# Kernel optimization log

Measured on AMD Instinct MI355X. Metric: run time of the kernel, lower is better.

The kernel has to match this reference:

```python
import jax, jax.numpy as jnp
import numpy as np

BN_EPS = 1e-5


def setup_inputs() -> dict:
    key = jax.random.key(0)
    ks = jax.random.split(key, 8)
    N, C, H, W = 16, 64, 56, 56
    Ch = C // 2
    x = jax.random.normal(ks[0], (N, C, H, W), dtype=jnp.float32)
    # 1x1 convs represented as [out, in] matrices
    w1 = jax.random.normal(ks[1], (Ch, C), dtype=jnp.float32) / np.sqrt(C)
    b1 = jnp.zeros((Ch,), dtype=jnp.float32)
    w2 = jax.random.normal(ks[2], (Ch, C), dtype=jnp.float32) / np.sqrt(C)
    b2 = jnp.zeros((Ch,), dtype=jnp.float32)
    w3 = jax.random.normal(ks[3], (C, C), dtype=jnp.float32) / np.sqrt(C)
    b3 = jnp.zeros((C,), dtype=jnp.float32)
    gamma = jnp.ones((C,), dtype=jnp.float32)
    beta = jnp.zeros((C,), dtype=jnp.float32)
    return {"x": x, "w1": w1, "b1": b1, "w2": w2, "b2": b2,
            "w3": w3, "b3": b3, "gamma": gamma, "beta": beta}


def _conv1x1(x, w, b):
    # x: [N,C,H,W], w: [O,C] -> [N,O,H,W]
    return jnp.einsum('nchw,oc->nohw', x, w) + b[None, :, None, None]


def reference(x, w1, b1, w2, b2, w3, b3, gamma, beta):
    N, C, H, W = x.shape
    S = H * W
    theta = _conv1x1(x, w1, b1)            # [N, C/2, H, W]
    phi = _conv1x1(x, w2, b2)              # [N, C/2, H, W]
    g = x                                  # [N, C, H, W]
    th = theta.reshape(N, -1, S)           # [N, C/2, S]
    ph = phi.reshape(N, -1, S)             # [N, C/2, S]
    gf = g.reshape(N, C, S)                # [N, C, S]
    scale = 1.0 / jnp.sqrt(jnp.float32(th.shape[1]))
    attn = jnp.einsum('nis,nit->nst', th, ph) * scale   # [N, S, S]
    attn = jax.nn.softmax(attn, axis=-1)
    f = jnp.einsum('nst,nit->nis', attn, gf).reshape(N, C, H, W)
    f = _conv1x1(f, w3, b3)
    # BatchNorm2d, training mode (batch statistics, biased variance)
    mean = jnp.mean(f, axis=(0, 2, 3), keepdims=True)
    var = jnp.mean((f - mean) ** 2, axis=(0, 2, 3), keepdims=True)
    f = (f - mean) / jnp.sqrt(var + BN_EPS)
    f = f * gamma[None, :, None, None] + beta[None, :, None, None]
    return x + f
```

## Files before the change

kernel.cpp:

```cpp
#include <hip/hip_runtime.h>
#include <hip/hip_bf16.h>

constexpr int N_ = 16, C_ = 64, CH_ = 32;
constexpr int S_ = 3136;
constexpr int SB = 64;
constexpr int NB = S_ / SB;
constexpr float SCALE = 0.17677669529663687f;
constexpr float LOG2E = 1.4426950408889634f;
constexpr float SCALE2 = SCALE * LOG2E;
constexpr float FIXM2 = 16.0f * LOG2E;

using f32x4 = __attribute__((ext_vector_type(4))) float;
using f32x16 = __attribute__((ext_vector_type(16))) float;
using bf16x8 = __attribute__((ext_vector_type(8))) short;
using u32x2 = __attribute__((ext_vector_type(2))) unsigned;
using u32x4 = __attribute__((ext_vector_type(4))) unsigned;

__device__ __forceinline__ unsigned cvtpk(float lo, float hi) {
  unsigned r;
  asm("v_cvt_pk_bf16_f32 %0, %1, %2" : "=v"(r) : "v"(lo), "v"(hi));
  return r;
}
__device__ __forceinline__ float exp2a(float x) {
  float r;
  asm("v_exp_f32 %0, %1" : "=v"(r) : "v"(x));
  return r;
}
__device__ __forceinline__ unsigned short f2bf(float f) {
  unsigned int u = __builtin_bit_cast(unsigned int, f);
  u += 0x7fffu + ((u >> 16) & 1u);
  return (unsigned short)(u >> 16);
}

__global__ __launch_bounds__(256)
void prep_kernel(const float* __restrict__ x,
                 const float* __restrict__ w1, const float* __restrict__ b1,
                 const float* __restrict__ w2, const float* __restrict__ b2,
                 unsigned short* __restrict__ thetaT,
                 unsigned short* __restrict__ phiT,
                 unsigned short* __restrict__ xbf) {
  __shared__ float xl[64][68];
  __shared__ __align__(16) unsigned short thL[64][40];
  __shared__ __align__(16) unsigned short phL[64][40];
  const int b = blockIdx.x;
  const int n = b / NB;
  const int s0 = (b % NB) * SB;
  const int tid = threadIdx.x;
  const int sl = tid & 63;
  const int grp = tid >> 6;

#pragma unroll
  for (int cc = 0; cc < 4; ++cc) {
    int c = cc * 16 + grp * 4 + (sl >> 4);
    int s4 = (sl & 15) * 4;
    size_t gidx = (size_t)(n * C_ + c) * S_ + s0 + s4;
    f32x4 v = *(const f32x4*)(x + gidx);
    *(f32x4*)&xl[c][s4] = v;
    u32x2 pb;
    pb.x = cvtpk(v[0], v[1]);
    pb.y = cvtpk(v[2], v[3]);
    *(u32x2*)(xbf + gidx) = pb;
  }
  __syncthreads();

  float acc1[8], acc2[8];
  const int i0u = __builtin_amdgcn_readfirstlane(grp * 8);
  const float* w1b = w1 + i0u * C_;
  const float* w2b = w2 + i0u * C_;
#pragma unroll
  for (int ii = 0; ii < 8; ++ii) {
    acc1[ii] = b1[i0u + ii];
    acc2[ii] = b2[i0u + ii];
  }
#pragma unroll 1
  for (int cc = 0; cc < 4; ++cc) {
    float xv[16];
#pragma unroll
    for (int k = 0; k < 16; ++k) xv[k] = xl[cc * 16 + k][sl];
#pragma unroll
    for (int ii = 0; ii < 8; ++ii) {
#pragma unroll
      for (int k = 0; k < 16; ++k) {
        acc1[ii] = fmaf(w1b[ii * C_ + cc * 16 + k], xv[k], acc1[ii]);
        acc2[ii] = fmaf(w2b[ii * C_ + cc * 16 + k], xv[k], acc2[ii]);
      }
    }
  }
  {
    u32x4 t4, p4;
    t4.x = cvtpk(acc1[0] * SCALE2, acc1[1] * SCALE2);
    t4.y = cvtpk(acc1[2] * SCALE2, acc1[3] * SCALE2);
    t4.z = cvtpk(acc1[4] * SCALE2, acc1[5] * SCALE2);
    t4.w = cvtpk(acc1[6] * SCALE2, acc1[7] * SCALE2);
    p4.x = cvtpk(acc2[0], acc2[1]);
    p4.y = cvtpk(acc2[2], acc2[3]);
    p4.z = cvtpk(acc2[4], acc2[5]);
    p4.w = cvtpk(acc2[6], acc2[7]);
    *(u32x4*)&thL[sl][grp * 8] = t4;
    *(u32x4*)&phL[sl][grp * 8] = p4;
  }
  __syncthreads();
  {
    int row = tid >> 2, ch = (tid & 3) * 8;
    size_t o = ((size_t)(n * S_) + s0 + row) * CH_ + ch;
    *(bf16x8*)(thetaT + o) = *(const bf16x8*)&thL[row][ch];
    *(bf16x8*)(phiT + o)   = *(const bf16x8*)&phL[row][ch];
  }
}

__global__ __launch_bounds__(256)
void attn_kernel(const unsigned short* __restrict__ thetaT,
                 const unsigned short* __restrict__ phiT,
                 const unsigned short* __restrict__ xbf,
                 const float* __restrict__ w3, const float* __restrict__ b3,
                 unsigned short* __restrict__ yb, float* __restrict__ partials) {
  __shared__ __align__(16) unsigned short ldsK[2][64 * 40];
  __shared__ __align__(16) unsigned short ldsV[2][64 * 72];
  __shared__ float redS[2][128];
  const int b = (blockIdx.x & 7) * 98 + (blockIdx.x >> 3);
  const int n = b / NB;
  const int q0 = (b % NB) * SB;
  const int tid = threadIdx.x;
  const int lane = tid & 63;
  const int w = tid >> 6;
  const int qw = w & 1;
  const int th = w >> 1;
  const int cl = lane & 31;
  const int h = lane >> 5;

  const unsigned short* thQ =
      thetaT + ((size_t)(n * S_) + q0 + qw * 32 + cl) * CH_;
  const bf16x8 qfA = *(const bf16x8*)(thQ + h * 8);
  const bf16x8 qfB = *(const bf16x8*)(thQ + 16 + h * 8);

  f32x16 oacc[2];
#pragma unroll
  for (int cb = 0; cb < 2; ++cb)
#pragma unroll
    for (int r = 0; r < 16; ++r) oacc[cb][r] = 0.f;
  float lsum = 0.f;
  f32x16 cinit;
#pragma unroll
  for (int r = 0; r < 16; ++r) cinit[r] = -FIXM2;

  const unsigned short* phiB = phiT + (size_t)n * S_ * CH_;
  const unsigned short* vB = xbf + (size_t)n * C_ * S_;

  const int krow = tid >> 2, kch = (tid & 3) * 8;
  const int vc = tid >> 3, vch = (tid & 7) * 8;

  bf16x8 kst, vst0, vst1;
  kst = *(const bf16x8*)(phiB + (size_t)krow * CH_ + kch);
  vst0 = *(const bf16x8*)(vB + (size_t)vc * S_ + vch);
  vst1 = *(const bf16x8*)(vB + (size_t)(vc + 32) * S_ + vch);
  *(bf16x8*)(ldsK[0] + krow * 40 + kch) = kst;
  *(bf16x8*)(ldsV[0] + vc * 72 + vch) = vst0;
  *(bf16x8*)(ldsV[0] + (vc + 32) * 72 + vch) = vst1;
  __syncthreads();

  int cur = 0;
#pragma unroll 1
  for (int t0 = 0; t0 < S_; t0 += 64) {
    const bool pre = (t0 + 64 < S_);
    if (pre) {
      kst = *(const bf16x8*)(phiB + (size_t)(t0 + 64 + krow) * CH_ + kch);
      vst0 = *(const bf16x8*)(vB + (size_t)vc * S_ + t0 + 64 + vch);
      vst1 = *(const bf16x8*)(vB + (size_t)(vc + 32) * S_ + t0 + 64 + vch);
    }

    const unsigned short* Kc = ldsK[cur];
    const unsigned short* Vc = ldsV[cur];

    const unsigned short* kr = Kc + (th * 32 + cl) * 40 + h * 8;
    bf16x8 kfA = *(const bf16x8*)(kr);
    bf16x8 kfB = *(const bf16x8*)(kr + 16);
    __builtin_amdgcn_s_setprio(1);
    f32x16 st = __builtin_amdgcn_mfma_f32_32x32x16_bf16(kfA, qfA, cinit, 0, 0, 0);
    st = __builtin_amdgcn_mfma_f32_32x32x16_bf16(kfB, qfB, st, 0, 0, 0);
    __builtin_amdgcn_s_setprio(0);

    float p[16];
#pragma unroll
    for (int r = 0; r < 16; ++r) {
      p[r] = exp2a(st[r]);
      lsum += p[r];
    }
    unsigned pkw[8];
#pragma unroll
    for (int i = 0; i < 8; ++i) pkw[i] = cvtpk(p[2 * i], p[2 * i + 1]);

    __builtin_amdgcn_s_setprio(1);
#pragma unroll
    for (int tb = 0; tb < 2; ++tb) {
      bf16x8 pf = __builtin_bit_cast(bf16x8,
          (u32x4){pkw[tb * 4 + 0], pkw[tb * 4 + 1], pkw[tb * 4 + 2], pkw[tb * 4 + 3]});
#pragma unroll
      for (int cb = 0; cb < 2; ++cb) {
        const unsigned short* vr =
            Vc + (cb * 32 + cl) * 72 + th * 32 + tb * 16 + 4 * h;
        u32x2 v0 = *(const u32x2*)(vr);
        u32x2 v1 = *(const u32x2*)(vr + 8);
        bf16x8 vf = __builtin_bit_cast(bf16x8, (u32x4){v0.x, v0.y, v1.x, v1.y});
        oacc[cb] = __builtin_amdgcn_mfma_f32_32x32x16_bf16(vf, pf, oacc[cb], 0, 0, 0);
      }
    }
    __builtin_amdgcn_s_setprio(0);

    if (pre) {
      *(bf16x8*)(ldsK[cur ^ 1] + krow * 40 + kch) = kst;
      *(bf16x8*)(ldsV[cur ^ 1] + vc * 72 + vch) = vst0;
      *(bf16x8*)(ldsV[cur ^ 1] + (vc + 32) * 72 + vch) = vst1;
    }
    __syncthreads();
    cur ^= 1;
  }

  float* mrg = (float*)&ldsV[0][0];
  if (th == 1) {
    float* pm = mrg + ((size_t)(qw * 64 + lane)) * 36;
#pragma unroll
    for (int cb = 0; cb < 2; ++cb)
#pragma unroll
      for (int i = 0; i < 4; ++i) {
        f32x4 v = {oacc[cb][4 * i], oacc[cb][4 * i + 1],
                   oacc[cb][4 * i + 2], oacc[cb][4 * i + 3]};
        *(f32x4*)(pm + cb * 16 + 4 * i) = v;
      }
    pm[32] = lsum;
  }
  __syncthreads();
  if (th == 0) {
    float* pm = mrg + ((size_t)(qw * 64 + lane)) * 36;
#pragma unroll
    for (int cb = 0; cb < 2; ++cb)
#pragma unroll
      for (int i = 0; i < 4; ++i) {
        f32x4 v = *(const f32x4*)(pm + cb * 16 + 4 * i);
        oacc[cb][4 * i] += v[0];
        oacc[cb][4 * i + 1] += v[1];
        oacc[cb][4 * i + 2] += v[2];
        oacc[cb][4 * i + 3] += v[3];
      }
    lsum += pm[32];

    float lt = lsum;
    lt += __shfl_xor(lt, 32);
    const float inv = 1.0f / lt;

    unsigned ff[4][4];
#pragma unroll
    for (int kb = 0; kb < 4; ++kb) {
      const int blk = kb >> 1, rb = (kb & 1) * 8;
#pragma unroll
      for (int i = 0; i < 4; ++i)
        ff[kb][i] = cvtpk(oacc[blk][rb + 2 * i] * inv,
                          oacc[blk][rb + 2 * i + 1] * inv);
    }

    const int q = q0 + qw * 32 + cl;
#pragma unroll
    for (int ch32 = 0; ch32 < 2; ++ch32) {
      const float* wr = w3 + (ch32 * 32 + cl) * C_;
      f32x16 acc;
      {
        f32x4 b0 = *(const f32x4*)(b3 + ch32 * 32 + 4 * h);
        f32x4 b1v = *(const f32x4*)(b3 + ch32 * 32 + 8 + 4 * h);
        f32x4 b2v = *(const f32x4*)(b3 + ch32 * 32 + 16 + 4 * h);
        f32x4 b3v = *(const f32x4*)(b3 + ch32 * 32 + 24 + 4 * h);
#pragma unroll
        for (int i = 0; i < 4; ++i) {
          acc[i] = b0[i];
          acc[4 + i] = b1v[i];
          acc[8 + i] = b2v[i];
          acc[12 + i] = b3v[i];
        }
      }
#pragma unroll
      for (int kb = 0; kb < 4; ++kb) {
        f32x4 a0 = *(const f32x4*)(wr + kb * 16 + 4 * h);
        f32x4 a1 = *(const f32x4*)(wr + kb * 16 + 8 + 4 * h);
        u32x4 wf;
        wf.x = cvtpk(a0[0], a0[1]);
        wf.y = cvtpk(a0[2], a0[3]);
        wf.z = cvtpk(a1[0], a1[1]);
        wf.w = cvtpk(a1[2], a1[3]);
        bf16x8 fb = __builtin_bit_cast(bf16x8,
            (u32x4){ff[kb][0], ff[kb][1], ff[kb][2], ff[kb][3]});
        acc = __builtin_amdgcn_mfma_f32_32x32x16_bf16(
            __builtin_bit_cast(bf16x8, wf), fb, acc, 0, 0, 0);
      }
#pragma unroll
      for (int r = 0; r < 16; ++r) {
        const int co = ch32 * 32 + (r & 3) + 8 * (r >> 2) + 4 * h;
        float yv = acc[r];
        yb[(size_t)(n * C_ + co) * S_ + q] = f2bf(yv);
        float s1 = yv, s2 = yv * yv;
#pragma unroll
        for (int off = 1; off < 32; off <<= 1) {
          s1 += __shfl_xor(s1, off);
          s2 += __shfl_xor(s2, off);
        }
        if (cl == 0) {
          redS[qw][co] = s1;
          redS[qw][64 + co] = s2;
        }
      }
    }
  }
  __syncthreads();
  if (tid < 128)
    partials[(size_t)b * 128 + tid] = redS[0][tid] + redS[1][tid];
}

__global__ __launch_bounds__(256)
void stats_kernel(const float* __restrict__ partials, float* __restrict__ stats) {
  __shared__ float red[4];
  const int c = blockIdx.x;
  const int tid = threadIdx.x;
  float s = 0.f;
  for (int r = tid; r < N_ * NB; r += 256) s += partials[(size_t)r * 128 + c];
#pragma unroll
  for (int off = 1; off < 64; off <<= 1) s += __shfl_xor(s, off);
  if ((tid & 63) == 0) red[tid >> 6] = s;
  __syncthreads();
  if (tid == 0) stats[c] = red[0] + red[1] + red[2] + red[3];
}

__global__ __launch_bounds__(256)
void bn_kernel(const unsigned short* __restrict__ xbf,
               const unsigned short* __restrict__ yb,
               const float* __restrict__ stats,
               const float* __restrict__ gamma, const float* __restrict__ beta,
               float* __restrict__ out) {
  const int idx = blockIdx.x * 256 + threadIdx.x;
  const size_t base = (size_t)idx * 8;
  const int c = (int)((base / S_) & 63);
  constexpr float invcnt = 1.0f / (N_ * S_);
  float mean = stats[c] * invcnt;
  float var = stats[64 + c] * invcnt - mean * mean;
  float a = gamma[c] * rsqrtf(var + 1e-5f);
  float bb = beta[c] - mean * a;
  u32x4 yv = *(const u32x4*)(yb + base);
  u32x4 xv = *(const u32x4*)(xbf + base);
#pragma unroll
  for (int hh = 0; hh < 2; ++hh) {
    f32x4 o;
#pragma unroll
    for (int r = 0; r < 2; ++r) {
      const int wsel = hh * 2 + r;
      unsigned py = (wsel == 0) ? yv.x : (wsel == 1) ? yv.y : (wsel == 2) ? yv.z : yv.w;
      unsigned px = (wsel == 0) ? xv.x : (wsel == 1) ? xv.y : (wsel == 2) ? xv.z : xv.w;
      float ylo = __builtin_bit_cast(float, py << 16);
      float yhi = __builtin_bit_cast(float, py & 0xffff0000u);
      float xlo = __builtin_bit_cast(float, px << 16);
      float xhi = __builtin_bit_cast(float, px & 0xffff0000u);
      o[r * 2 + 0] = fmaf(ylo, a, xlo + bb);
      o[r * 2 + 1] = fmaf(yhi, a, xhi + bb);
    }
    *(f32x4*)(out + base + hh * 4) = o;
  }
}

extern "C" void kernel_launch(void* const* d_in, const int* in_sizes, int n_in,
                              void* d_out, int out_size, void* d_ws, size_t ws_size,
                              hipStream_t stream) {
  const float* x = (const float*)d_in[0];
  const float* w1 = (const float*)d_in[1];
  const float* b1 = (const float*)d_in[2];
  const float* w2 = (const float*)d_in[3];
  const float* b2 = (const float*)d_in[4];
  const float* w3 = (const float*)d_in[5];
  const float* b3 = (const float*)d_in[6];
  const float* gamma = (const float*)d_in[7];
  const float* beta = (const float*)d_in[8];

  char* ws = (char*)d_ws;
  unsigned short* thetaT = (unsigned short*)(ws + 0);
  unsigned short* phiT   = (unsigned short*)(ws + 3211264);
  unsigned short* xbf    = (unsigned short*)(ws + 6422528);
  unsigned short* yb     = (unsigned short*)(ws + 12845056);
  float* stats           = (float*)(ws + 19267584);
  float* partials        = (float*)(ws + 19268096);
  if (ws_size < 19669504) return;

  prep_kernel<<<N_ * NB, 256, 0, stream>>>(x, w1, b1, w2, b2, thetaT, phiT, xbf);
  attn_kernel<<<N_ * NB, 256, 0, stream>>>(thetaT, phiT, xbf, w3, b3, yb, partials);
  stats_kernel<<<128, 256, 0, stream>>>(partials, stats);
  bn_kernel<<<(out_size / 8) / 256, 256, 0, stream>>>(xbf, yb, stats, gamma, beta, (float*)d_out);
}
```

Measured before the change: 105.0 us.

## Load K and V fragments straight from global into registers, dropping LDS staging

The attention loop no longer stages phi (K) and x (V) tiles through double-buffered shared memory. Each lane now loads its MFMA fragments directly from global memory into registers, with a two-stage register ping-pong prefetch, which removes the per-iteration __syncthreads and the LDS traffic. The cost is more global load instructions with narrower 8-byte V accesses and redundant loads across waves, which now depend on L1/L2 hits. Register pressure also rises, which may lower occupancy.

```diff
diff --git a/kernel.cpp b/kernel.cpp
--- a/kernel.cpp
+++ b/kernel.cpp
@@ -114,8 +114,7 @@
                  const unsigned short* __restrict__ xbf,
                  const float* __restrict__ w3, const float* __restrict__ b3,
                  unsigned short* __restrict__ yb, float* __restrict__ partials) {
-  __shared__ __align__(16) unsigned short ldsK[2][64 * 40];
-  __shared__ __align__(16) unsigned short ldsV[2][64 * 72];
+  __shared__ float mrg[2][64][36];
   __shared__ float redS[2][128];
   const int b = (blockIdx.x & 7) * 98 + (blockIdx.x >> 3);
   const int n = b / NB;
@@ -143,42 +142,32 @@
 #pragma unroll
   for (int r = 0; r < 16; ++r) cinit[r] = -FIXM2;
 
-  const unsigned short* phiB = phiT + (size_t)n * S_ * CH_;
-  const unsigned short* vB = xbf + (size_t)n * C_ * S_;
-
-  const int krow = tid >> 2, kch = (tid & 3) * 8;
-  const int vc = tid >> 3, vch = (tid & 7) * 8;
-
-  bf16x8 kst, vst0, vst1;
-  kst = *(const bf16x8*)(phiB + (size_t)krow * CH_ + kch);
-  vst0 = *(const bf16x8*)(vB + (size_t)vc * S_ + vch);
-  vst1 = *(const bf16x8*)(vB + (size_t)(vc + 32) * S_ + vch);
-  *(bf16x8*)(ldsK[0] + krow * 40 + kch) = kst;
-  *(bf16x8*)(ldsV[0] + vc * 72 + vch) = vst0;
-  *(bf16x8*)(ldsV[0] + (vc + 32) * 72 + vch) = vst1;
-  __syncthreads();
-
-  int cur = 0;
-#pragma unroll 1
-  for (int t0 = 0; t0 < S_; t0 += 64) {
-    const bool pre = (t0 + 64 < S_);
-    if (pre) {
-      kst = *(const bf16x8*)(phiB + (size_t)(t0 + 64 + krow) * CH_ + kch);
-      vst0 = *(const bf16x8*)(vB + (size_t)vc * S_ + t0 + 64 + vch);
-      vst1 = *(const bf16x8*)(vB + (size_t)(vc + 32) * S_ + t0 + 64 + vch);
-    }
-
-    const unsigned short* Kc = ldsK[cur];
-    const unsigned short* Vc = ldsV[cur];
-
-    const unsigned short* kr = Kc + (th * 32 + cl) * 40 + h * 8;
-    bf16x8 kfA = *(const bf16x8*)(kr);
-    bf16x8 kfB = *(const bf16x8*)(kr + 16);
+  const unsigned short* kBase =
+      phiT + (size_t)n * S_ * CH_ + (size_t)(th * 32 + cl) * CH_ + h * 8;
+  const unsigned short* vBase =
+      xbf + (size_t)n * C_ * S_ + (size_t)cl * S_ + th * 32 + 4 * h;
+  const size_t vRow32 = (size_t)32 * S_;
+
+  bf16x8 kA0, kB0, kA1, kB1;
+  u32x2 VA[8], VB[8];
+
+  auto prefetch = [&](bf16x8& KA, bf16x8& KB, u32x2* VV, int t) {
+    const unsigned short* kp = kBase + (size_t)t * CH_;
+    KA = *(const bf16x8*)kp;
+    KB = *(const bf16x8*)(kp + 16);
+    const unsigned short* vp = vBase + t;
+#pragma unroll
+    for (int j = 0; j < 4; ++j) VV[j] = *(const u32x2*)(vp + j * 8);
+    const unsigned short* vp2 = vp + vRow32;
+#pragma unroll
+    for (int j = 0; j < 4; ++j) VV[4 + j] = *(const u32x2*)(vp2 + j * 8);
+  };
+
+  auto compute = [&](bf16x8 KA, bf16x8 KB, const u32x2* VV) {
     __builtin_amdgcn_s_setprio(1);
-    f32x16 st = __builtin_amdgcn_mfma_f32_32x32x16_bf16(kfA, qfA, cinit, 0, 0, 0);
-    st = __builtin_amdgcn_mfma_f32_32x32x16_bf16(kfB, qfB, st, 0, 0, 0);
+    f32x16 st = __builtin_amdgcn_mfma_f32_32x32x16_bf16(KA, qfA, cinit, 0, 0, 0);
+    st = __builtin_amdgcn_mfma_f32_32x32x16_bf16(KB, qfB, st, 0, 0, 0);
     __builtin_amdgcn_s_setprio(0);
-
     float p[16];
 #pragma unroll
     for (int r = 0; r < 16; ++r) {
@@ -188,7 +177,6 @@
     unsigned pkw[8];
 #pragma unroll
     for (int i = 0; i < 8; ++i) pkw[i] = cvtpk(p[2 * i], p[2 * i + 1]);
-
     __builtin_amdgcn_s_setprio(1);
 #pragma unroll
     for (int tb = 0; tb < 2; ++tb) {
@@ -196,28 +184,28 @@
           (u32x4){pkw[tb * 4 + 0], pkw[tb * 4 + 1], pkw[tb * 4 + 2], pkw[tb * 4 + 3]});
 #pragma unroll
       for (int cb = 0; cb < 2; ++cb) {
-        const unsigned short* vr =
-            Vc + (cb * 32 + cl) * 72 + th * 32 + tb * 16 + 4 * h;
-        u32x2 v0 = *(const u32x2*)(vr);
-        u32x2 v1 = *(const u32x2*)(vr + 8);
+        u32x2 v0 = VV[cb * 4 + tb * 2];
+        u32x2 v1 = VV[cb * 4 + tb * 2 + 1];
         bf16x8 vf = __builtin_bit_cast(bf16x8, (u32x4){v0.x, v0.y, v1.x, v1.y});
         oacc[cb] = __builtin_amdgcn_mfma_f32_32x32x16_bf16(vf, pf, oacc[cb], 0, 0, 0);
       }
     }
     __builtin_amdgcn_s_setprio(0);
-
-    if (pre) {
-      *(bf16x8*)(ldsK[cur ^ 1] + krow * 40 + kch) = kst;
-      *(bf16x8*)(ldsV[cur ^ 1] + vc * 72 + vch) = vst0;
-      *(bf16x8*)(ldsV[cur ^ 1] + (vc + 32) * 72 + vch) = vst1;
-    }
-    __syncthreads();
-    cur ^= 1;
-  }
-
-  float* mrg = (float*)&ldsV[0][0];
+  };
+
+  prefetch(kA0, kB0, VA, 0);
+#pragma unroll 1
+  for (int i = 0; i < 24; ++i) {
+    const int t = i * 128;
+    prefetch(kA1, kB1, VB, t + 64);
+    compute(kA0, kB0, VA);
+    prefetch(kA0, kB0, VA, t + 128);
+    compute(kA1, kB1, VB);
+  }
+  compute(kA0, kB0, VA);
+
   if (th == 1) {
-    float* pm = mrg + ((size_t)(qw * 64 + lane)) * 36;
+    float* pm = &mrg[qw][lane][0];
 #pragma unroll
     for (int cb = 0; cb < 2; ++cb)
 #pragma unroll
@@ -230,7 +218,7 @@
   }
   __syncthreads();
   if (th == 0) {
-    float* pm = mrg + ((size_t)(qw * 64 + lane)) * 36;
+    float* pm = &mrg[qw][lane][0];
 #pragma unroll
     for (int cb = 0; cb < 2; ++cb)
 #pragma unroll
```

After: 243.3 us. 2.32x slower.
